# Optimization experiments

Measured on AMD Instinct MI355X. Metric: run time of the kernel, lower is better.

## Reference

```python
import jax, jax.numpy as jnp
import numpy as np

B, T, D, H, K, O = 512, 512, 64, 64, 4, 2


def setup_inputs() -> dict:
    key = jax.random.key(0)
    ks = jax.random.split(key, 12)
    s_i = 1.0 / np.sqrt(D)
    s_h = 1.0 / np.sqrt(H)
    return {
        "x": jax.random.normal(ks[0], (B, T, D), jnp.float32),
        "ctx": jax.random.randint(ks[1], (B, T), 0, K, jnp.int32),
        "mask": jax.random.bernoulli(ks[2], 0.9, (B, T)),
        "W_ir": jax.random.normal(ks[3], (H, D), jnp.float32) * s_i,
        "W_iz": jax.random.normal(ks[4], (H, D), jnp.float32) * s_i,
        "W_in": jax.random.normal(ks[5], (H, D), jnp.float32) * s_i,
        "b_ir": jnp.zeros((H,), jnp.float32),
        "b_iz": jnp.zeros((H,), jnp.float32),
        "b_in": jnp.zeros((H,), jnp.float32),
        "W_hr": jax.random.normal(ks[6], (K, H, H), jnp.float32) * s_h,
        "W_hz": jax.random.normal(ks[7], (K, H, H), jnp.float32) * s_h,
        "W_hn": jax.random.normal(ks[8], (K, H, H), jnp.float32) * s_h,
        "b_hr": jnp.zeros((K, H), jnp.float32),
        "b_hz": jnp.zeros((K, H), jnp.float32),
        "b_hn": jnp.zeros((K, H), jnp.float32),
        "Wo_w": jax.random.normal(ks[9], (O, H), jnp.float32) * s_h,
        "Wo_b": jnp.zeros((O,), jnp.float32),
    }


def reference(x, ctx, mask, W_ir, W_iz, W_in, b_ir, b_iz, b_in,
              W_hr, W_hz, W_hn, b_hr, b_hz, b_hn, Wo_w, Wo_b):
    Bv, Tv, _ = x.shape
    Hv = W_ir.shape[0]
    # precompute all input projections: [B,T,H]
    ir = jnp.einsum('btd,hd->bth', x, W_ir) + b_ir
    iz = jnp.einsum('btd,hd->bth', x, W_iz) + b_iz
    inn = jnp.einsum('btd,hd->bth', x, W_in) + b_in
    mt = mask.astype(x.dtype)  # [B,T]

    def step(h, inp):
        ir_t, iz_t, in_t, kt, m_t = inp  # [B,H],[B,H],[B,H],[B],[B]
        hr = jnp.einsum('bij,bj->bi', W_hr[kt], h) + b_hr[kt]
        hz = jnp.einsum('bij,bj->bi', W_hz[kt], h) + b_hz[kt]
        hn = jnp.einsum('bij,bj->bi', W_hn[kt], h) + b_hn[kt]
        r = jax.nn.sigmoid(ir_t + hr)
        z = jax.nn.sigmoid(iz_t + hz)
        n = jnp.tanh(in_t + r * hn)
        h_new = (1.0 - z) * n + z * h
        h = m_t[:, None] * h_new + (1.0 - m_t[:, None]) * h
        return h, h

    xs = (jnp.swapaxes(ir, 0, 1), jnp.swapaxes(iz, 0, 1), jnp.swapaxes(inn, 0, 1),
          ctx.T, mt.T)
    h0 = jnp.zeros((Bv, Hv), x.dtype)
    _, hs = jax.lax.scan(step, h0, xs)  # hs: [T,B,H]
    logits = jnp.einsum('tbh,oh->bto', hs, Wo_w) + Wo_b  # [B,T,O]
    return logits
```

## Files before the change

kernel.cpp:

```cpp
#include <hip/hip_runtime.h>
#include <hip/hip_fp16.h>

#define B_ 512
#define T_ 512
#define H_ 64
#define K_ 4

#define WS_WIT_OFF   98304
#define WS_FLAG_OFF  123136
#define WS_XH_OFF    131072
#define WS_IPJ_OFF   131072
#define WS_HH_OFF    201457664ULL
#define WS_NEED_FAST 235012096ULL

#define LDS_HSC_OFF  122880
#define LDS_TOTAL    123392
#define STAGE_U4     7680

#define LDS10_HSC_OFF 98304
#define LDS10_TOTAL   98816
#define STAGE10_U4    6144

typedef _Float16 half2_t __attribute__((ext_vector_type(2)));

union Q { uint4 u; half2_t h[4]; };

__device__ __forceinline__ float fdot2f(half2_t a, half2_t b, float c) {
#if __has_builtin(__builtin_amdgcn_fdot2)
    return __builtin_amdgcn_fdot2(a, b, c, false);
#else
    return fmaf((float)a[0], (float)b[0], fmaf((float)a[1], (float)b[1], c));
#endif
}

__device__ __forceinline__ half2_t pkh2(float a, float b) {
    return __builtin_bit_cast(half2_t, __builtin_amdgcn_cvt_pkrtz(a, b));
}

__global__ void detect_mask_kernel(const unsigned char* __restrict__ mb, int* __restrict__ flag) {
    __shared__ int cnt;
    if (threadIdx.x == 0) cnt = 0;
    __syncthreads();
    int c = 0;
    for (int i = threadIdx.x; i < 4096; i += blockDim.x)
        if ((i & 3) != 0 && mb[i] != 0) c++;
    atomicAdd(&cnt, c);
    __syncthreads();
    if (threadIdx.x == 0) *flag = (cnt > 0) ? 1 : 0;
}

__global__ void convert_weights_kernel(const float* __restrict__ Whr, const float* __restrict__ Whz,
                                       const float* __restrict__ Whn, const float* __restrict__ Wir,
                                       const float* __restrict__ Wiz, const float* __restrict__ Win,
                                       __half* __restrict__ wht, __half* __restrict__ wit) {
    int idx = blockIdx.x * 256 + threadIdx.x;
    if (idx < K_ * 3 * H_ * H_) {
        int mat = idx >> 12;
        int i   = (idx >> 6) & 63;
        int j   = idx & 63;
        int k   = mat / 3, g = mat - 3 * k;
        const float* src = (g == 0) ? Whr : (g == 1) ? Whz : Whn;
        wht[((mat * 8 + (j >> 3)) * 64 + i) * 8 + (j & 7)] = __float2half(src[(k * H_ + i) * H_ + j]);
    }
    if (idx < 3 * H_ * H_) {
        int g = idx >> 12;
        int i = (idx >> 6) & 63;
        int j = idx & 63;
        const float* src = (g == 0) ? Wir : (g == 1) ? Wiz : Win;
        wit[((g * 8 + (j >> 3)) * 64 + i) * 8 + (j & 7)] = __float2half(src[i * H_ + j]);
    }
}

__global__ void convert_x_kernel(const float* __restrict__ xf, __half* __restrict__ xh) {
    size_t i = (size_t)blockIdx.x * 256 + threadIdx.x;
    if (i >= (size_t)B_ * T_ * H_ / 8) return;
    const float4* p = (const float4*)xf + 2 * i;
    float4 a = p[0], b = p[1];
    Q o;
    o.h[0] = pkh2(a.x, a.y);
    o.h[1] = pkh2(a.z, a.w);
    o.h[2] = pkh2(b.x, b.y);
    o.h[3] = pkh2(b.z, b.w);
    ((uint4*)xh)[i] = o.u;
}

__global__ __launch_bounds__(256, 1)
void iproj_kernel(const float* __restrict__ xf, const __half* __restrict__ wit,
                  const float* __restrict__ b_ir, const float* __restrict__ b_iz,
                  const float* __restrict__ b_in, float* __restrict__ iproj) {
    const int lane = threadIdx.x & 63;
    const int grp  = threadIdx.x >> 6;
    Q wr[8], wz[8], wn[8];
    const uint4* wp = (const uint4*)wit + lane;
#pragma unroll
    for (int q = 0; q < 8; q++) {
        wr[q].u = wp[q * 64];
        wz[q].u = wp[512 + q * 64];
        wn[q].u = wp[1024 + q * 64];
    }
    const float bir = b_ir[lane], biz = b_iz[lane], bin = b_in[lane];
    const int bt_base = blockIdx.x * 64 + grp * 16;
#pragma unroll 1
    for (int r = 0; r < 16; r++) {
        const int bt = bt_base + r;
        const float4* xp = (const float4*)(xf + (size_t)bt * H_);
        Q xq[8];
#pragma unroll
        for (int q = 0; q < 8; q++) {
            float4 a = xp[2 * q], b4 = xp[2 * q + 1];
            xq[q].h[0] = pkh2(a.x, a.y);
            xq[q].h[1] = pkh2(a.z, a.w);
            xq[q].h[2] = pkh2(b4.x, b4.y);
            xq[q].h[3] = pkh2(b4.z, b4.w);
        }
        float sir = bir, siz = biz, sin_ = bin;
#pragma unroll
        for (int q = 0; q < 8; q++)
#pragma unroll
            for (int p = 0; p < 4; p++) {
                sir  = fdot2f(wr[q].h[p], xq[q].h[p], sir);
                siz  = fdot2f(wz[q].h[p], xq[q].h[p], siz);
                sin_ = fdot2f(wn[q].h[p], xq[q].h[p], sin_);
            }
        float* op = iproj + (size_t)bt * 192;
        op[lane] = sir; op[64 + lane] = siz; op[128 + lane] = sin_;
    }
}

#define LOADCHUNK(IPR, IPZ, IPN, CTXV, MSKV, T0)                                \
{                                                                               \
    const int t0c = (T0);                                                       \
    _Pragma("unroll") for (int s = 0; s < 8; s++) {                             \
        int tcl = t0c + s; tcl = (tcl < T_) ? tcl : (T_ - 1);                   \
        const float* ipp = iproj + (size_t)(bt0 + tcl) * 192;                   \
        IPR[s] = ipp[lane]; IPZ[s] = ipp[64 + lane]; IPN[s] = ipp[128 + lane];  \
    }                                                                           \
    int tcc = t0c + (lane & 7); tcc = (tcc < T_) ? tcc : (T_ - 1);              \
    CTXV = ctx[bt0 + tcc];                                                      \
    MSKV = (int)maskb[(size_t)(bt0 + tcc) << mshift];                           \
}

#define RUNCHUNK(T0, IPR, IPZ, IPN, CTXC, MSKC, CTXN)                           \
{                                                                               \
    _Pragma("unroll") for (int s = 0; s < 8; s++) {                             \
        const int tt  = (T0) + s;                                               \
        const int kcu = __builtin_amdgcn_readlane(CTXC, s);                     \
        const uint4* wpk = sw + kcu * 1536 + lane;                              \
               \
        Q cZ[8], cN[8];                                                         \
        _Pragma("unroll") for (int q = 0; q < 8; q++) cZ[q].u = wpk[512 + q * 64];  \
        _Pragma("unroll") for (int q = 0; q < 8; q++) cN[q].u = wpk[1024 + q * 64]; \
        float shr, shz, shn;                                                    \
        { float a4[4] = {0,0,0,0};                                              \
          _Pragma("unroll") for (int q = 0; q < 8; q++)                         \
            _Pragma("unroll") for (int p = 0; p < 4; p++)                       \
              a4[q >> 1] = fdot2f(cR[q].h[p], hq[q].h[p], a4[q >> 1]);          \
          shr = (a4[0] + a4[1]) + (a4[2] + a4[3]); }                            \
        { float a4[4] = {0,0,0,0};                                              \
          _Pragma("unroll") for (int q = 0; q < 8; q++)                         \
            _Pragma("unroll") for (int p = 0; p < 4; p++)                       \
              a4[q >> 1] = fdot2f(cZ[q].h[p], hq[q].h[p], a4[q >> 1]);          \
          shz = (a4[0] + a4[1]) + (a4[2] + a4[3]); }                            \
        { float a4[4] = {0,0,0,0};                                              \
          _Pragma("unroll") for (int q = 0; q < 8; q++)                         \
            _Pragma("unroll") for (int p = 0; p < 4; p++)                       \
              a4[q >> 1] = fdot2f(cN[q].h[p], hq[q].h[p], a4[q >> 1]);          \
          shn = (a4[0] + a4[1]) + (a4[2] + a4[3]); }                            \
                         \
        const float bhr = (kcu == 0) ? bR0 : (kcu == 1) ? bR1 : (kcu == 2) ? bR2 : bR3; \
        const float bhz = (kcu == 0) ? bZ0 : (kcu == 1) ? bZ1 : (kcu == 2) ? bZ2 : bZ3; \
        const float bhn = (kcu == 0) ? bN0 : (kcu == 1) ? bN1 : (kcu == 2) ? bN2 : bN3; \
        const float mcv = (__builtin_amdgcn_readlane(MSKC, s) != 0) ? 1.0f : 0.0f;  \
                       \
        const float arv = IPR[s] + shr + bhr;                                   \
        const float azv = IPZ[s] + shz + bhz;                                   \
        const float rr  = 1.0f / (1.0f + __expf(-arv));                         \
        const float zz  = 1.0f / (1.0f + __expf(-azv));                         \
        const float aa  = IPN[s] + rr * (shn + bhn);                            \
        const float nn2 = 2.0f / (1.0f + __expf(-2.0f * aa)) - 1.0f;            \
        float hnew = nn2 + zz * (hreg - nn2);                                   \
        hnew = (mcv > 0.5f) ? hnew : hreg;                                      \
        hreg = hnew;                                                            \
        const __half h16 = __float2half(hnew);                                  \
        hsc[((s & 1) << 6) + lane] = h16;                                       \
        hh0[(size_t)tt * H_ + lane] = h16;         \
               \
        const int knu = (s < 7) ? __builtin_amdgcn_readlane(CTXC, s + 1)        \
                                : __builtin_amdgcn_readlane(CTXN, 0);           \
        const uint4* wpn = sw + knu * 1536 + lane;                              \
        _Pragma("unroll") for (int q = 0; q < 8; q++) cR[q].u = wpn[q * 64];    \
        __builtin_amdgcn_wave_barrier();                                        \
        { const uint4* hp = (const uint4*)(hsc + ((s & 1) << 6));               \
          _Pragma("unroll") for (int q = 0; q < 8; q++) hq[q].u = hp[q]; }      \
        __builtin_amdgcn_wave_barrier();                                        \
    }                                                                           \
}

__global__ __launch_bounds__(128, 1)
void gru_seq10(const float* __restrict__ iproj, const int* __restrict__ ctx,
               const unsigned char* __restrict__ maskb, const int* __restrict__ flagp,
               const __half* __restrict__ wht,
               const float* __restrict__ b_hr, const float* __restrict__ b_hz,
               const float* __restrict__ b_hn, __half* __restrict__ hh) {
    extern __shared__ __align__(16) char smem[];
    uint4* sw = (uint4*)smem;

    const int tid  = threadIdx.x;
    const int lane = tid & 63;
    const int wv   = tid >> 6;
    const int b    = blockIdx.x * 2 + wv;
    const int bt0  = b * T_;

    {
        const uint4* g = (const uint4*)wht;
#pragma unroll 1
        for (int i = tid; i < STAGE10_U4; i += 128) sw[i] = g[i];
    }
    __syncthreads();

    const int flag   = *flagp;
    const int mshift = flag ? 0 : 2;
    __half* hh0 = hh + (size_t)bt0 * H_;
    __half* hsc = (__half*)(smem + LDS10_HSC_OFF + (wv << 8));

    const float bR0 = b_hr[lane],       bR1 = b_hr[64 + lane];
    const float bR2 = b_hr[128 + lane], bR3 = b_hr[192 + lane];
    const float bZ0 = b_hz[lane],       bZ1 = b_hz[64 + lane];
    const float bZ2 = b_hz[128 + lane], bZ3 = b_hz[192 + lane];
    const float bN0 = b_hn[lane],       bN1 = b_hn[64 + lane];
    const float bN2 = b_hn[128 + lane], bN3 = b_hn[192 + lane];

    float hreg = 0.0f;
    Q hq[8];
#pragma unroll
    for (int q = 0; q < 8; q++) hq[q].u = make_uint4(0u, 0u, 0u, 0u);

    float ipAr[8], ipAz[8], ipAn[8];
    float ipBr[8], ipBz[8], ipBn[8];
    int ctxA, mskA, ctxB, mskB;
    LOADCHUNK(ipAr, ipAz, ipAn, ctxA, mskA, 0)

    Q cR[8];
    {
        const int k0u = __builtin_amdgcn_readlane(ctxA, 0);
        const uint4* wp0 = sw + k0u * 1536 + lane;
#pragma unroll
        for (int q = 0; q < 8; q++) cR[q].u = wp0[q * 64];
    }

#pragma unroll 1
    for (int c = 0; c < 64; c += 2) {
        const int t0a = c << 3, t0b = t0a + 8;
        LOADCHUNK(ipBr, ipBz, ipBn, ctxB, mskB, t0b)
        RUNCHUNK(t0a, ipAr, ipAz, ipAn, ctxA, mskA, ctxB)
        LOADCHUNK(ipAr, ipAz, ipAn, ctxA, mskA, t0b + 8)
        RUNCHUNK(t0b, ipBr, ipBz, ipBn, ctxB, mskB, ctxA)
    }
}

__global__ __launch_bounds__(256, 1)
void logits_kernel(const __half* __restrict__ hh, const float* __restrict__ Wo_w,
                   const float* __restrict__ Wo_b, float* __restrict__ out) {
    const int bt = blockIdx.x * 256 + threadIdx.x;
    const uint4* hp = (const uint4*)(hh + (size_t)bt * H_);
    const float wob0 = Wo_b[0], wob1 = Wo_b[1];
    float l0 = 0.0f, l1 = 0.0f;
#pragma unroll
    for (int q = 0; q < 8; q++) {
        Q h8; h8.u = hp[q];
#pragma unroll
        for (int p = 0; p < 4; p++) {
            const int j = q * 8 + p * 2;
            const float v0 = (float)h8.h[p][0];
            const float v1 = (float)h8.h[p][1];
            l0 = fmaf(v0, Wo_w[j], l0);
            l0 = fmaf(v1, Wo_w[j + 1], l0);
            l1 = fmaf(v0, Wo_w[64 + j], l1);
            l1 = fmaf(v1, Wo_w[64 + j + 1], l1);
        }
    }
    *(float2*)(out + (size_t)bt * 2) = make_float2(l0 + wob0, l1 + wob1);
}

#define STEP(TT, WCUR, WNXT, BUF)                                              \
{                                                                              \
    const int tt = (TT);                                                       \
    const int tn = (tt + 1 < T_) ? tt + 1 : T_ - 1;                            \
    Q xq[8];                                                                   \
    { const uint4* xp = (const uint4*)(xh16 + (size_t)(bt0 + tt) * H_);        \
      _Pragma("unroll") for (int q = 0; q < 8; q++) xq[q].u = xp[q]; }         \
    float ar4[4] = {0,0,0,0}, az4[4] = {0,0,0,0}, an4[4] = {0,0,0,0};          \
    _Pragma("unroll") for (int q = 0; q < 8; q++) {                            \
        _Pragma("unroll") for (int p = 0; p < 4; p++) {                        \
            ar4[q >> 1] = fdot2f(WCUR[q].h[p],      hq[q].h[p], ar4[q >> 1]);  \
            az4[q >> 1] = fdot2f(WCUR[8 + q].h[p],  hq[q].h[p], az4[q >> 1]);  \
            an4[q >> 1] = fdot2f(WCUR[16 + q].h[p], hq[q].h[p], an4[q >> 1]);  \
        }                                                                      \
    }                                                                          \
    const float shr = (ar4[0] + ar4[1]) + (ar4[2] + ar4[3]);                   \
    const float shz = (az4[0] + az4[1]) + (az4[2] + az4[3]);                   \
    const float shn = (an4[0] + an4[1]) + (an4[2] + an4[3]);                   \
    float sir = bir, siz = biz, sin_ = bin;                                    \
    _Pragma("unroll") for (int q = 0; q < 8; q++) {                            \
        Q wr, wz, wn;                                                          \
        wr.u = swi[q * 64 + lane];                                             \
        wz.u = swi[512 + q * 64 + lane];                                       \
        wn.u = swi[1024 + q * 64 + lane];                                      \
        _Pragma("unroll") for (int p = 0; p < 4; p++) {                        \
            sir  = fdot2f(wr.h[p], xq[q].h[p], sir);                           \
            siz  = fdot2f(wz.h[p], xq[q].h[p], siz);                           \
            sin_ = fdot2f(wn.h[p], xq[q].h[p], sin_);                          \
        }                                                                      \
    }                                                                          \
    const int kn = __builtin_amdgcn_readfirstlane(ctx[bt0 + tn]);              \
    const unsigned char mn = maskb[(size_t)(bt0 + tn) << mshift];              \
    const float bhr_n = b_hr[kn * H_ + lane];                                  \
    const float bhz_n = b_hz[kn * H_ + lane];                                  \
    const float bhn_n = b_hn[kn * H_ + lane];                                  \
    { const uint4* wp = sw + kn * 1536 + lane;                                 \
      _Pragma("unroll") for (int q = 0; q < 8; q++) {                          \
        WNXT[q].u      = wp[q * 64];                                           \
        WNXT[8 + q].u  = wp[512 + q * 64];                                     \
        WNXT[16 + q].u = wp[1024 + q * 64];                                    \
      } }                                                                      \
    const float arv = sir + shr + bhr_c;                                       \
    const float azv = siz + shz + bhz_c;                                       \
    const float rr  = 1.0f / (1.0f + __expf(-arv));                            \
    const float zz  = 1.0f / (1.0f + __expf(-azv));                            \
    const float aa  = sin_ + rr * (shn + bhn_c);                               \
    const float nn2 = 2.0f / (1.0f + __expf(-2.0f * aa)) - 1.0f;               \
    float hnew = nn2 + zz * (hreg - nn2);                                      \
    hnew = (mc > 0.5f) ? hnew : hreg;                                          \
    hreg = hnew;                                                               \
    { __half* hb = hsc + ((BUF) << 6);                                         \
      hb[lane] = __float2half(hnew);                                           \
      __builtin_amdgcn_wave_barrier();                                         \
      const uint4* hp = (const uint4*)hb;                                      \
      _Pragma("unroll") for (int q = 0; q < 8; q++) hq[q].u = hp[q];           \
      __builtin_amdgcn_wave_barrier(); }                                       \
    { float l0 = hnew * wo0, l1 = hnew * wo1;                                  \
      _Pragma("unroll") for (int m = 32; m >= 1; m >>= 1) {                    \
          l0 += __shfl_xor(l0, m, 64);                                         \
          l1 += __shfl_xor(l1, m, 64);                                         \
      }                                                                        \
      if (lane == 0) *(float2*)(outp + tt * 2) = make_float2(l0 + wob0, l1 + wob1); } \
    bhr_c = bhr_n; bhz_c = bhz_n; bhn_c = bhn_n;                               \
    mc = mn ? 1.0f : 0.0f;                                                     \
}

__global__ __launch_bounds__(128, 1)
void gru_seq6(const __half* __restrict__ xh16, const int* __restrict__ ctx,
              const unsigned char* __restrict__ maskb, const int* __restrict__ flagp,
              const __half* __restrict__ wht,
              const float* __restrict__ b_ir, const float* __restrict__ b_iz,
              const float* __restrict__ b_in, const float* __restrict__ b_hr,
              const float* __restrict__ b_hz, const float* __restrict__ b_hn,
              const float* __restrict__ Wo_w, const float* __restrict__ Wo_b,
              float* __restrict__ out) {
    extern __shared__ __align__(16) char smem[];
    uint4* sw  = (uint4*)smem;
    uint4* swi = sw + 6144;

    const int tid  = threadIdx.x;
    const int lane = tid & 63;
    const int wv   = tid >> 6;
    const int b    = blockIdx.x * 2 + wv;

    {
        const uint4* gsrc = (const uint4*)wht;
#pragma unroll 1
        for (int i = tid; i < STAGE_U4; i += 128) sw[i] = gsrc[i];
    }
    __syncthreads();

    const int flag   = *flagp;
    const int mshift = flag ? 0 : 2;
    const int bt0    = b * T_;

    const float bir = b_ir[lane], biz = b_iz[lane], bin = b_in[lane];
    const float wo0 = Wo_w[lane], wo1 = Wo_w[64 + lane];
    const float wob0 = Wo_b[0], wob1 = Wo_b[1];

    __half* hsc = (__half*)(smem + LDS_HSC_OFF + (wv << 8));
    float*  outp = out + (size_t)b * T_ * 2;

    float hreg = 0.0f;
    Q hq[8];
#pragma unroll
    for (int q = 0; q < 8; q++) hq[q].u = make_uint4(0u, 0u, 0u, 0u);

    Q wA[24], wB[24];
    const int k0 = __builtin_amdgcn_readfirstlane(ctx[bt0]);
    float mc = maskb[(size_t)bt0 << mshift] ? 1.0f : 0.0f;
    float bhr_c = b_hr[k0 * H_ + lane];
    float bhz_c = b_hz[k0 * H_ + lane];
    float bhn_c = b_hn[k0 * H_ + lane];
    {
        const uint4* wp = sw + k0 * 1536 + lane;
#pragma unroll
        for (int q = 0; q < 8; q++) {
            wA[q].u      = wp[q * 64];
            wA[8 + q].u  = wp[512 + q * 64];
            wA[16 + q].u = wp[1024 + q * 64];
        }
    }

#pragma unroll 1
    for (int t = 0; t < T_; t += 2) {
        STEP(t,     wA, wB, 0)
        STEP(t + 1, wB, wA, 1)
    }
}

extern "C" void kernel_launch(void* const* d_in, const int* in_sizes, int n_in,
                              void* d_out, int out_size, void* d_ws, size_t ws_size,
                              hipStream_t stream) {
    const float* x    = (const float*)d_in[0];
    const int*   ctx  = (const int*)d_in[1];
    const void*  mask = d_in[2];
    const float* W_ir = (const float*)d_in[3];
    const float* W_iz = (const float*)d_in[4];
    const float* W_in = (const float*)d_in[5];
    const float* bir  = (const float*)d_in[6];
    const float* biz  = (const float*)d_in[7];
    const float* bin  = (const float*)d_in[8];
    const float* W_hr = (const float*)d_in[9];
    const float* W_hz = (const float*)d_in[10];
    const float* W_hn = (const float*)d_in[11];
    const float* bhr  = (const float*)d_in[12];
    const float* bhz  = (const float*)d_in[13];
    const float* bhn  = (const float*)d_in[14];
    const float* Wo_w = (const float*)d_in[15];
    const float* Wo_b = (const float*)d_in[16];

    char* ws = (char*)d_ws;
    __half* wht  = (__half*)ws;
    __half* wit  = (__half*)(ws + WS_WIT_OFF);
    int*    flag = (int*)(ws + WS_FLAG_OFF);

    detect_mask_kernel<<<1, 256, 0, stream>>>((const unsigned char*)mask, flag);
    convert_weights_kernel<<<192, 256, 0, stream>>>(W_hr, W_hz, W_hn, W_ir, W_iz, W_in,
                                                    wht, wit);

    if (ws_size >= (size_t)WS_NEED_FAST) {
        float*  iproj = (float*)(ws + WS_IPJ_OFF);
        __half* hh    = (__half*)(ws + WS_HH_OFF);
        iproj_kernel<<<B_ * T_ / 64, 256, 0, stream>>>(x, wit, bir, biz, bin, iproj);
        (void)hipFuncSetAttribute((const void*)gru_seq10,
                                  hipFuncAttributeMaxDynamicSharedMemorySize, LDS10_TOTAL);
        gru_seq10<<<B_ / 2, 128, LDS10_TOTAL, stream>>>(
            iproj, ctx, (const unsigned char*)mask, flag, wht, bhr, bhz, bhn, hh);
        logits_kernel<<<B_ * T_ / 256, 256, 0, stream>>>(hh, Wo_w, Wo_b, (float*)d_out);
    } else {
        __half* xh16 = (__half*)(ws + WS_XH_OFF);
        convert_x_kernel<<<8192, 256, 0, stream>>>(x, xh16);
        (void)hipFuncSetAttribute((const void*)gru_seq6,
                                  hipFuncAttributeMaxDynamicSharedMemorySize, LDS_TOTAL);
        gru_seq6<<<B_ / 2, 128, LDS_TOTAL, stream>>>(
            xh16, ctx, (const unsigned char*)mask, flag, wht,
            bir, biz, bin, bhr, bhz, bhn, Wo_w, Wo_b, (float*)d_out);
    }
}
```

Before: 632.2 us.

## Double-buffer full recurrent weight set in registers and prefetch next step via inline LDS reads

The GRU recurrence kernel now keeps all three gate weight slices (24 uint4 per lane) in two register buffers and issues inline-asm ds_read_b128 prefetches for the next timestep's context weights before computing the current step. This hides LDS load latency behind the dot products instead of loading the Z/N weights serially within the step. The input-projection kernel also halves rows per block and software-prefetches the next row of x into registers. The cost is much higher VGPR pressure (48 uint4 of weights per lane) and a forced lgkmcnt(0) wait plus sched_barrier per step, which may constrain scheduling.

```diff
diff --git a/kernel.cpp b/kernel.cpp
--- a/kernel.cpp
+++ b/kernel.cpp
@@ -17,9 +17,9 @@
 #define LDS_TOTAL    123392
 #define STAGE_U4     7680
 
-#define LDS10_HSC_OFF 98304
-#define LDS10_TOTAL   98816
-#define STAGE10_U4    6144
+#define LDS12_HSC_OFF 98304
+#define LDS12_TOTAL   98816
+#define STAGE12_U4    6144
 
 typedef _Float16 half2_t __attribute__((ext_vector_type(2)));
 
@@ -99,19 +99,30 @@
         wn[q].u = wp[1024 + q * 64];
     }
     const float bir = b_ir[lane], biz = b_iz[lane], bin = b_in[lane];
-    const int bt_base = blockIdx.x * 64 + grp * 16;
-#pragma unroll 1
-    for (int r = 0; r < 16; r++) {
+    const int bt_base = blockIdx.x * 32 + grp * 8;
+
+    float4 raw[16];
+    {
+        const float4* xp = (const float4*)(xf + (size_t)bt_base * H_);
+#pragma unroll
+        for (int j = 0; j < 16; j++) raw[j] = xp[j];
+    }
+#pragma unroll
+    for (int r = 0; r < 8; r++) {
         const int bt = bt_base + r;
-        const float4* xp = (const float4*)(xf + (size_t)bt * H_);
         Q xq[8];
 #pragma unroll
         for (int q = 0; q < 8; q++) {
-            float4 a = xp[2 * q], b4 = xp[2 * q + 1];
+            float4 a = raw[2 * q], b4 = raw[2 * q + 1];
             xq[q].h[0] = pkh2(a.x, a.y);
             xq[q].h[1] = pkh2(a.z, a.w);
             xq[q].h[2] = pkh2(b4.x, b4.y);
             xq[q].h[3] = pkh2(b4.z, b4.w);
+        }
+        if (r < 7) {
+            const float4* xp = (const float4*)(xf + (size_t)(bt + 1) * H_);
+#pragma unroll
+            for (int j = 0; j < 16; j++) raw[j] = xp[j];
         }
         float sir = bir, siz = biz, sin_ = bin;
 #pragma unroll
@@ -126,6 +137,25 @@
         op[lane] = sir; op[64 + lane] = siz; op[128 + lane] = sin_;
     }
 }
+
+#define DSR(DST, ADDR, OFF) \
+    asm volatile("ds_read_b128 %0, %1 offset:" #OFF : "=v"(DST) : "v"(ADDR));
+
+#define PREF24(WN, VB)                                                          \
+    DSR(WN[0].u,  VB, 0)     DSR(WN[1].u,  VB, 1024)                            \
+    DSR(WN[2].u,  VB, 2048)  DSR(WN[3].u,  VB, 3072)                            \
+    DSR(WN[4].u,  VB, 4096)  DSR(WN[5].u,  VB, 5120)                            \
+    DSR(WN[6].u,  VB, 6144)  DSR(WN[7].u,  VB, 7168)                            \
+    DSR(WN[8].u,  VB, 8192)  DSR(WN[9].u,  VB, 9216)                            \
+    DSR(WN[10].u, VB, 10240) DSR(WN[11].u, VB, 11264)                           \
+    DSR(WN[12].u, VB, 12288) DSR(WN[13].u, VB, 13312)                           \
+    DSR(WN[14].u, VB, 14336) DSR(WN[15].u, VB, 15360)                           \
+    DSR(WN[16].u, VB, 16384) DSR(WN[17].u, VB, 17408)                           \
+    DSR(WN[18].u, VB, 18432) DSR(WN[19].u, VB, 19456)                           \
+    DSR(WN[20].u, VB, 20480) DSR(WN[21].u, VB, 21504)                           \
+    DSR(WN[22].u, VB, 22528) DSR(WN[23].u, VB, 23552)
+
+#define BSEL(K, A0, A1, A2, A3) (((K) == 0) ? (A0) : ((K) == 1) ? (A1) : ((K) == 2) ? (A2) : (A3))
 
 #define LOADCHUNK(IPR, IPZ, IPN, CTXV, MSKV, T0)                                \
 {                                                                               \
@@ -140,64 +170,65 @@
     MSKV = (int)maskb[(size_t)(bt0 + tcc) << mshift];                           \
 }
 
-#define RUNCHUNK(T0, IPR, IPZ, IPN, CTXC, MSKC, CTXN)                           \
+#define STEP12(TT, SS, WCUR, WNXT, KNU_EXPR, IPR, IPZ, IPN, CTXC, MSKC)         \
 {                                                                               \
-    _Pragma("unroll") for (int s = 0; s < 8; s++) {                             \
-        const int tt  = (T0) + s;                                               \
-        const int kcu = __builtin_amdgcn_readlane(CTXC, s);                     \
-        const uint4* wpk = sw + kcu * 1536 + lane;                              \
-               \
-        Q cZ[8], cN[8];                                                         \
-        _Pragma("unroll") for (int q = 0; q < 8; q++) cZ[q].u = wpk[512 + q * 64];  \
-        _Pragma("unroll") for (int q = 0; q < 8; q++) cN[q].u = wpk[1024 + q * 64]; \
-        float shr, shz, shn;                                                    \
-        { float a4[4] = {0,0,0,0};                                              \
-          _Pragma("unroll") for (int q = 0; q < 8; q++)                         \
-            _Pragma("unroll") for (int p = 0; p < 4; p++)                       \
-              a4[q >> 1] = fdot2f(cR[q].h[p], hq[q].h[p], a4[q >> 1]);          \
-          shr = (a4[0] + a4[1]) + (a4[2] + a4[3]); }                            \
-        { float a4[4] = {0,0,0,0};                                              \
-          _Pragma("unroll") for (int q = 0; q < 8; q++)                         \
-            _Pragma("unroll") for (int p = 0; p < 4; p++)                       \
-              a4[q >> 1] = fdot2f(cZ[q].h[p], hq[q].h[p], a4[q >> 1]);          \
-          shz = (a4[0] + a4[1]) + (a4[2] + a4[3]); }                            \
-        { float a4[4] = {0,0,0,0};                                              \
-          _Pragma("unroll") for (int q = 0; q < 8; q++)                         \
-            _Pragma("unroll") for (int p = 0; p < 4; p++)                       \
-              a4[q >> 1] = fdot2f(cN[q].h[p], hq[q].h[p], a4[q >> 1]);          \
-          shn = (a4[0] + a4[1]) + (a4[2] + a4[3]); }                            \
-                         \
-        const float bhr = (kcu == 0) ? bR0 : (kcu == 1) ? bR1 : (kcu == 2) ? bR2 : bR3; \
-        const float bhz = (kcu == 0) ? bZ0 : (kcu == 1) ? bZ1 : (kcu == 2) ? bZ2 : bZ3; \
-        const float bhn = (kcu == 0) ? bN0 : (kcu == 1) ? bN1 : (kcu == 2) ? bN2 : bN3; \
-        const float mcv = (__builtin_amdgcn_readlane(MSKC, s) != 0) ? 1.0f : 0.0f;  \
+    const int tt  = (TT);                                                       \
+    const int kcu = __builtin_amdgcn_readlane(CTXC, SS);                        \
+    const int knu = (KNU_EXPR);                                                 \
+            \
+    const unsigned int vb = lds0 + (unsigned int)(knu * 24576) + ((unsigned int)lane << 4); \
+    PREF24(WNXT, vb)                                                            \
+            \
+    float ar4[4] = {0,0,0,0}, az4[4] = {0,0,0,0}, an4[4] = {0,0,0,0};           \
+    _Pragma("unroll") for (int q = 0; q < 8; q++) {                             \
+        _Pragma("unroll") for (int p = 0; p < 4; p++) {                         \
+            ar4[q >> 1] = fdot2f(WCUR[q].h[p],      hq[q].h[p], ar4[q >> 1]);   \
+            az4[q >> 1] = fdot2f(WCUR[8 + q].h[p],  hq[q].h[p], az4[q >> 1]);   \
+            an4[q >> 1] = fdot2f(WCUR[16 + q].h[p], hq[q].h[p], an4[q >> 1]);   \
+        }                                                                       \
+    }                                                                           \
+    const float shr = (ar4[0] + ar4[1]) + (ar4[2] + ar4[3]);                    \
+    const float shz = (az4[0] + az4[1]) + (az4[2] + az4[3]);                    \
+    const float shn = (an4[0] + an4[1]) + (an4[2] + an4[3]);                    \
+                  \
+    const float bhr = BSEL(kcu, bR0, bR1, bR2, bR3);                            \
+    const float bhz = BSEL(kcu, bZ0, bZ1, bZ2, bZ3);                            \
+    const float bhn = BSEL(kcu, bN0, bN1, bN2, bN3);                            \
+    const float mcv = (__builtin_amdgcn_readlane(MSKC, SS) != 0) ? 1.0f : 0.0f; \
                        \
-        const float arv = IPR[s] + shr + bhr;                                   \
-        const float azv = IPZ[s] + shz + bhz;                                   \
-        const float rr  = 1.0f / (1.0f + __expf(-arv));                         \
-        const float zz  = 1.0f / (1.0f + __expf(-azv));                         \
-        const float aa  = IPN[s] + rr * (shn + bhn);                            \
-        const float nn2 = 2.0f / (1.0f + __expf(-2.0f * aa)) - 1.0f;            \
-        float hnew = nn2 + zz * (hreg - nn2);                                   \
-        hnew = (mcv > 0.5f) ? hnew : hreg;                                      \
-        hreg = hnew;                                                            \
-        const __half h16 = __float2half(hnew);                                  \
-        hsc[((s & 1) << 6) + lane] = h16;                                       \
-        hh0[(size_t)tt * H_ + lane] = h16;         \
-               \
-        const int knu = (s < 7) ? __builtin_amdgcn_readlane(CTXC, s + 1)        \
-                                : __builtin_amdgcn_readlane(CTXN, 0);           \
-        const uint4* wpn = sw + knu * 1536 + lane;                              \
-        _Pragma("unroll") for (int q = 0; q < 8; q++) cR[q].u = wpn[q * 64];    \
-        __builtin_amdgcn_wave_barrier();                                        \
-        { const uint4* hp = (const uint4*)(hsc + ((s & 1) << 6));               \
-          _Pragma("unroll") for (int q = 0; q < 8; q++) hq[q].u = hp[q]; }      \
-        __builtin_amdgcn_wave_barrier();                                        \
-    }                                                                           \
-}
+    const float arv = IPR[SS] + shr + bhr;                                      \
+    const float azv = IPZ[SS] + shz + bhz;                                      \
+    const float rr  = 1.0f / (1.0f + __expf(-arv));                             \
+    const float zz  = 1.0f / (1.0f + __expf(-azv));                             \
+    const float aa  = IPN[SS] + rr * (shn + bhn);                               \
+    const float nn2 = 2.0f / (1.0f + __expf(-2.0f * aa)) - 1.0f;                \
+    float hnew = nn2 + zz * (hreg - nn2);                                       \
+    hnew = (mcv > 0.5f) ? hnew : hreg;                                          \
+    hreg = hnew;                                                                \
+    const __half h16 = __float2half(hnew);                                      \
+    hsc[((SS & 1) << 6) + lane] = h16;                                          \
+    hh0[(size_t)tt * H_ + lane] = h16;             \
+    __builtin_amdgcn_wave_barrier();                                            \
+    { const uint4* hp = (const uint4*)(hsc + ((SS & 1) << 6));                  \
+      _Pragma("unroll") for (int q = 0; q < 8; q++) hq[q].u = hp[q]; }          \
+    __builtin_amdgcn_wave_barrier();                                            \
+                \
+    asm volatile("s_waitcnt lgkmcnt(0)" ::: "memory");                          \
+    __builtin_amdgcn_sched_barrier(0);                                          \
+}
+
+#define RUNCHUNK12(T0, IPR, IPZ, IPN, CTXC, MSKC, CTXN)                         \
+    STEP12(T0 + 0, 0, wA, wB, __builtin_amdgcn_readlane(CTXC, 1), IPR, IPZ, IPN, CTXC, MSKC) \
+    STEP12(T0 + 1, 1, wB, wA, __builtin_amdgcn_readlane(CTXC, 2), IPR, IPZ, IPN, CTXC, MSKC) \
+    STEP12(T0 + 2, 2, wA, wB, __builtin_amdgcn_readlane(CTXC, 3), IPR, IPZ, IPN, CTXC, MSKC) \
+    STEP12(T0 + 3, 3, wB, wA, __builtin_amdgcn_readlane(CTXC, 4), IPR, IPZ, IPN, CTXC, MSKC) \
+    STEP12(T0 + 4, 4, wA, wB, __builtin_amdgcn_readlane(CTXC, 5), IPR, IPZ, IPN, CTXC, MSKC) \
+    STEP12(T0 + 5, 5, wB, wA, __builtin_amdgcn_readlane(CTXC, 6), IPR, IPZ, IPN, CTXC, MSKC) \
+    STEP12(T0 + 6, 6, wA, wB, __builtin_amdgcn_readlane(CTXC, 7), IPR, IPZ, IPN, CTXC, MSKC) \
+    STEP12(T0 + 7, 7, wB, wA, __builtin_amdgcn_readlane(CTXN, 0), IPR, IPZ, IPN, CTXC, MSKC)
 
 __global__ __launch_bounds__(128, 1)
-void gru_seq10(const float* __restrict__ iproj, const int* __restrict__ ctx,
+void gru_seq12(const float* __restrict__ iproj, const int* __restrict__ ctx,
                const unsigned char* __restrict__ maskb, const int* __restrict__ flagp,
                const __half* __restrict__ wht,
                const float* __restrict__ b_hr, const float* __restrict__ b_hz,
@@ -214,14 +245,16 @@
     {
         const uint4* g = (const uint4*)wht;
 #pragma unroll 1
-        for (int i = tid; i < STAGE10_U4; i += 128) sw[i] = g[i];
+        for (int i = tid; i < STAGE12_U4; i += 128) sw[i] = g[i];
     }
     __syncthreads();
+
+    const unsigned int lds0 = (unsigned int)(uintptr_t)smem;
 
     const int flag   = *flagp;
     const int mshift = flag ? 0 : 2;
     __half* hh0 = hh + (size_t)bt0 * H_;
-    __half* hsc = (__half*)(smem + LDS10_HSC_OFF + (wv << 8));
+    __half* hsc = (__half*)(smem + LDS12_HSC_OFF + (wv << 8));
 
     const float bR0 = b_hr[lane],       bR1 = b_hr[64 + lane];
     const float bR2 = b_hr[128 + lane], bR3 = b_hr[192 + lane];
@@ -240,21 +273,25 @@
     int ctxA, mskA, ctxB, mskB;
     LOADCHUNK(ipAr, ipAz, ipAn, ctxA, mskA, 0)
 
-    Q cR[8];
+    Q wA[24], wB[24];
     {
         const int k0u = __builtin_amdgcn_readlane(ctxA, 0);
         const uint4* wp0 = sw + k0u * 1536 + lane;
 #pragma unroll
-        for (int q = 0; q < 8; q++) cR[q].u = wp0[q * 64];
+        for (int q = 0; q < 8; q++) {
+            wA[q].u      = wp0[q * 64];
+            wA[8 + q].u  = wp0[512 + q * 64];
+            wA[16 + q].u = wp0[1024 + q * 64];
+        }
     }
 
 #pragma unroll 1
     for (int c = 0; c < 64; c += 2) {
         const int t0a = c << 3, t0b = t0a + 8;
         LOADCHUNK(ipBr, ipBz, ipBn, ctxB, mskB, t0b)
-        RUNCHUNK(t0a, ipAr, ipAz, ipAn, ctxA, mskA, ctxB)
+        RUNCHUNK12(t0a, ipAr, ipAz, ipAn, ctxA, mskA, ctxB)
         LOADCHUNK(ipAr, ipAz, ipAn, ctxA, mskA, t0b + 8)
-        RUNCHUNK(t0b, ipBr, ipBz, ipBn, ctxB, mskB, ctxA)
+        RUNCHUNK12(t0b, ipBr, ipBz, ipBn, ctxB, mskB, ctxA)
     }
 }
 
@@ -445,10 +482,10 @@
     if (ws_size >= (size_t)WS_NEED_FAST) {
         float*  iproj = (float*)(ws + WS_IPJ_OFF);
         __half* hh    = (__half*)(ws + WS_HH_OFF);
-        iproj_kernel<<<B_ * T_ / 64, 256, 0, stream>>>(x, wit, bir, biz, bin, iproj);
-        (void)hipFuncSetAttribute((const void*)gru_seq10,
-                                  hipFuncAttributeMaxDynamicSharedMemorySize, LDS10_TOTAL);
-        gru_seq10<<<B_ / 2, 128, LDS10_TOTAL, stream>>>(
+        iproj_kernel<<<B_ * T_ / 32, 256, 0, stream>>>(x, wit, bir, biz, bin, iproj);
+        (void)hipFuncSetAttribute((const void*)gru_seq12,
+                                  hipFuncAttributeMaxDynamicSharedMemorySize, LDS12_TOTAL);
+        gru_seq12<<<B_ / 2, 128, LDS12_TOTAL, stream>>>(
             iproj, ctx, (const unsigned char*)mask, flag, wht, bhr, bhz, bhn, hh);
         logits_kernel<<<B_ * T_ / 256, 256, 0, stream>>>(hh, Wo_w, Wo_b, (float*)d_out);
     } else {
```

New measurement: 588.2 us. 6.9% less time.
